# Optimization experiments

Measured on AMD Instinct MI355X. Metric: run time of the kernel, lower is better.

The kernel has to match this reference:

```python
import jax, jax.numpy as jnp
import numpy as np

H = 1024
E = 1024
B = 4096
DEPTH = 1


def setup_inputs() -> dict:
    key = jax.random.key(0)
    ks = jax.random.split(key, 12)
    s = 1.0 / np.sqrt(E + 2 * H)
    inp = {
        "X": jax.random.normal(ks[0], (B, E), jnp.float32),
        "index": 0,
        "length": 64,
        "prev_a": jax.random.normal(ks[1], (B, DEPTH + 1, H), jnp.float32),
        "prev_b": jax.random.normal(ks[2], (B, DEPTH + 1, H), jnp.float32),
        "prev_depth": jax.random.randint(ks[3], (B, 1), 0, 2, jnp.int32),
        # torch Linear weights: y = x @ W.T, W shape (out, in)
        "w_a00": jax.random.uniform(ks[4], (H, E + 2 * H), jnp.float32, -s, s),
        "w_a10": jax.random.uniform(ks[5], (H, E + H), jnp.float32, -s, s),
        "w_b00": jax.random.uniform(ks[6], (H, E + 2 * H), jnp.float32, -s, s),
        "w_b11": jax.random.uniform(ks[7], (H, E + H), jnp.float32, -s, s),
        "w_b10": jax.random.uniform(ks[8], (H, E + H), jnp.float32, -s, s),
        "w_b01": jax.random.uniform(ks[9], (H, E + 2 * H), jnp.float32, -s, s),
        "w_att": jax.random.uniform(ks[10], (4, 8 * H), jnp.float32, -s, s),
    }
    return inp


def _gate(pd, cond_val, branch, carry):
    # eq(pd,cond)*branch + gt(pd,cond)*carry + lt(pd,cond)*0
    eq = (pd == cond_val).astype(branch.dtype)
    gt = (pd > cond_val).astype(branch.dtype)
    return eq * branch + gt * carry


def reference(X, index, length, prev_a, prev_b, prev_depth,
              w_a00, w_a10, w_b00, w_b11, w_b10, w_b01, w_att):
    b, h = X.shape[0], prev_b.shape[-1]
    pd = prev_depth.astype(X.dtype)  # (B,1)
    a0, a1 = prev_a[:, 0, :], prev_a[:, 1, :]
    b0, b1 = prev_b[:, 0, :], prev_b[:, 1, :]

    # d = 1 (only depth level)
    nofork_nojoin_a = jnp.concatenate([X, b0, a1], 1) @ w_a00.T
    fork_nojoin_a = jnp.concatenate([X, b0], 1) @ w_a10.T
    na00 = _gate(pd, 1.0, nofork_nojoin_a, a1)
    na11 = _gate(pd, 1.0, a1, a1)                 # fork_join_a = prev_a[:,1]
    na10 = _gate(pd, 0.0, fork_nojoin_a, a1)      # eq(pd+1, 1) <=> pd == 0
    na01 = _gate(pd, 2.0, a0, a1)                 # eq(pd-1, 1) <=> pd == 2

    fork_join_b = jnp.concatenate([X, b1], 1) @ w_b11.T
    nofork_nojoin_b = jnp.concatenate([X, a1, na00], 1) @ w_b00.T
    fork_nojoin_b = jnp.concatenate([X, na10], 1) @ w_b10.T
    nofork_join_b = jnp.concatenate([X, b0, a1], 1) @ w_b01.T
    nb00 = _gate(pd, 1.0, nofork_nojoin_b, b1)
    nb11 = _gate(pd, 1.0, fork_join_b, b1)
    nb10 = _gate(pd, 0.0, fork_nojoin_b, b1)
    nb01 = _gate(pd, 2.0, nofork_join_b, b1)

    zeros2h = jnp.zeros((b, 2 * h), X.dtype)  # d=0 slot of each branch
    f00 = jnp.concatenate([zeros2h, na00, nb00], 1)  # (B, stride=4h)
    f01 = jnp.concatenate([zeros2h, na01, nb01], 1)
    f10 = jnp.concatenate([zeros2h, na10, nb10], 1)
    f11 = jnp.concatenate([zeros2h, na11, nb11], 1)
    state = jnp.stack([f00, f01, f10, f11], 1)  # (B, 4, 4h)

    # attention over next_state_flat[:, depth_size:] == [f10, f11]
    att_in = jnp.concatenate([f10, f11], 1)  # (B, 8h)
    pd0 = pd[:, 0]
    e0 = (pd0 == 0.0).astype(X.dtype)
    e1 = (pd0 == 1.0).astype(X.dtype)
    eD = (pd0 == float(DEPTH)).astype(X.dtype)
    mask = jnp.stack([1 - e0, (1 - e0) * (1 - e1), 1 - eD, 1 - e0], 1)  # (B,4)
    att_vars = mask * jax.nn.softmax(jax.nn.sigmoid(att_in @ w_att.T), axis=1)

    # straight-through argmax: forward one-hot, backward identity
    hard = jax.nn.one_hot(jnp.argmax(att_vars, axis=1), 4, dtype=X.dtype)
    sel = jax.lax.stop_gradient(hard - att_vars) + att_vars

    # bmm with striped identity == select the chosen stripe
    hidden = jnp.einsum('bk,bkd->bd', sel, state).reshape(b, DEPTH + 1, 2 * h)
    next_a = hidden[:, :, :h]
    next_b = hidden[:, :, h:]

    pdi = prev_depth[:, 0]
    hi = hard.astype(prev_depth.dtype)
    next_depth = (hi[:, 0] * pdi + hi[:, 1] * (pdi - 1)
                  + hi[:, 2] * (pdi + 1) + hi[:, 3] * pdi)[:, None]
    f = (sel[:, 2] + sel[:, 3])[:, None]
    j = (sel[:, 1] + sel[:, 3])[:, None]
    return (next_a, next_b, next_depth, f, j)
```

## Files before the change

### kernel.cpp

```cpp
#include <hip/hip_runtime.h>
#include <hip/hip_bf16.h>
#include <stdint.h>
#include <math.h>

typedef unsigned short u16;
typedef __attribute__((ext_vector_type(8))) short frag8;
typedef __attribute__((ext_vector_type(4))) float f32x4;

#define Hdim 1024
#define Brows 4096

#define OUT_B_OFF  8388608
#define OUT_D_OFF 16777216
#define OUT_F_OFF 16781312
#define OUT_J_OFF 16785408

#define XB      0u
#define B0B     4194304u
#define A1B     8388608u
#define B1B     12582912u
#define NA00B   16777216u
#define NA10B   20971520u
#define WA00B   25165824u
#define WA10B   28311552u
#define WB00B   30408704u
#define WB11B   33554432u
#define WB10B   35651584u
#define WS_BF_ELTS 37748736u
#define WS_NEED (32768ull + (unsigned long long)WS_BF_ELTS * 2ull)

#define NO_BCOPY 0xFFFFFFFFu

__device__ __forceinline__ u16 f2bf(float f) {
    union { float f; unsigned int i; } v; v.f = f;
    unsigned int r = v.i + 0x7fffu + ((v.i >> 16) & 1u);
    return (u16)(r >> 16);
}
__device__ __forceinline__ unsigned int pk2(float a, float b) {
    __hip_bfloat162 h = __float22bfloat162_rn(make_float2(a, b));
    union { __hip_bfloat162 h; unsigned int u; } v; v.h = h; return v.u;
}
__device__ __forceinline__ void gl_lds16(const u16* g, u16* l) {
    __builtin_amdgcn_global_load_lds(
        (const __attribute__((address_space(1))) unsigned int*)g,
        (__attribute__((address_space(3))) unsigned int*)l, 16, 0, 0);
}


struct GDesc {
    unsigned int a0, a1s, a2;
    unsigned int w;
    unsigned int bcopy;
    int K;
    int ksel;
    int pad;
    const int* gate;
    float* outp;
};
struct GPack { GDesc d[3]; };

__global__ __launch_bounds__(256)
void gemm_multi(u16* __restrict__ ws16, GPack gp)
{
    __shared__ alignas(16) u16 lsA[128 * 64];
    __shared__ alignas(16) u16 lsB[64 * 64];

    const GDesc g = gp.d[blockIdx.z];

    const int tid  = threadIdx.x;
    const int lane = tid & 63;
    const int wv   = tid >> 6;
    const int wm   = wv >> 1, wn = wv & 1;
    const int m0   = blockIdx.x * 128;
    const int n0   = blockIdx.y * 64;

    f32x4 acc[4][2];
#pragma unroll
    for (int i = 0; i < 4; ++i)
#pragma unroll
        for (int j = 0; j < 2; ++j) acc[i][j] = (f32x4){0.f, 0.f, 0.f, 0.f};

    const u16* segp[3] = { ws16 + g.a0, ws16 + g.a1s, ws16 + g.a2 };
    const u16* W = ws16 + g.w;
    const int K = g.K;

    const int nkt = K / 64;
    for (int kt = 0; kt < nkt; ++kt) {
        const int seg = kt >> 4;
        const int kl  = (kt & 15) * 64;
        const u16* ab = segp[seg] + (size_t)m0 * 1024 + kl;
        const u16* wb = W + (size_t)n0 * K + kt * 64;
#pragma unroll
        for (int i = 0; i < 4; ++i) {
            const int ch = i * 256 + tid;
            const int r = ch >> 3, c = ch & 7;
            gl_lds16(ab + (size_t)r * 1024 + ((c ^ (r & 7)) * 8), &lsA[ch * 8]);
        }
#pragma unroll
        for (int i = 0; i < 2; ++i) {
            const int ch = i * 256 + tid;
            const int r = ch >> 3, c = ch & 7;
            gl_lds16(wb + (size_t)r * K + ((c ^ (r & 7)) * 8), &lsB[ch * 8]);
        }
        __syncthreads();
#pragma unroll
        for (int ks = 0; ks < 2; ++ks) {
            const int kb = (ks * 32 + (lane >> 4) * 8) * 2;
            frag8 af[4], bfr[2];
#pragma unroll
            for (int i = 0; i < 4; ++i) {
                const int ro = wm * 64 + i * 16 + (lane & 15);
                af[i] = *(const frag8*)((const char*)lsA +
                            ((ro * 128 + kb) ^ ((ro & 7) << 4)));
            }
#pragma unroll
            for (int j = 0; j < 2; ++j) {
                const int ro = wn * 32 + j * 16 + (lane & 15);
                bfr[j] = *(const frag8*)((const char*)lsB +
                            ((ro * 128 + kb) ^ ((ro & 7) << 4)));
            }
#pragma unroll
            for (int i = 0; i < 4; ++i)
#pragma unroll
                for (int j = 0; j < 2; ++j)
                    acc[i][j] = __builtin_amdgcn_mfma_f32_16x16x32_bf16(af[i], bfr[j], acc[i][j], 0, 0, 0);
        }
        __syncthreads();
    }

    u16* bc = (g.bcopy != NO_BCOPY) ? (ws16 + g.bcopy) : nullptr;
    const int quad = lane >> 4;
    const int lcol = lane & 15;
#pragma unroll
    for (int i = 0; i < 4; ++i) {
#pragma unroll
        for (int r = 0; r < 4; ++r) {
            const int grow = m0 + wm * 64 + i * 16 + quad * 4 + r;
            const int gv = g.gate[grow];
#pragma unroll
            for (int j = 0; j < 2; ++j) {
                const int gcol = n0 + wn * 32 + j * 16 + lcol;
                const float v = acc[i][j][r];
                if (bc) bc[(size_t)grow * 1024 + gcol] = f2bf(v);
                if (gv == g.ksel) g.outp[(size_t)grow * 2048 + gcol] = v;
            }
        }
    }
}

__global__ __launch_bounds__(256)
void convert_all(const float* __restrict__ X,
                 const float* __restrict__ prev_a, const float* __restrict__ prev_b,
                 const float* __restrict__ wa00, const float* __restrict__ wa10,
                 const float* __restrict__ wb00, const float* __restrict__ wb11,
                 const float* __restrict__ wb10,
                 u16* __restrict__ ws16)
{
    long long gid = (long long)blockIdx.x * 256 + threadIdx.x;
    const float* src;
    unsigned int dst;
    long long idx;
    if (gid < 1048576) {
        idx = gid;               src = X + idx * 4;    dst = XB;
    } else if (gid < 1835008) {
        idx = gid - 1048576;     src = wa00 + idx * 4; dst = WA00B;
    } else if (gid < 2359296) {
        idx = gid - 1835008;     src = wa10 + idx * 4; dst = WA10B;
    } else if (gid < 3145728) {
        idx = gid - 2359296;     src = wb00 + idx * 4; dst = WB00B;
    } else if (gid < 3670016) {
        idx = gid - 3145728;     src = wb11 + idx * 4; dst = WB11B;
    } else if (gid < 4194304) {
        idx = gid - 3670016;     src = wb10 + idx * 4; dst = WB10B;
    } else if (gid < 5242880) {
        idx = gid - 4194304;
        src = prev_b + (idx >> 8) * 2048 + (idx & 255) * 4;          dst = B0B;
    } else if (gid < 6291456) {
        idx = gid - 5242880;
        src = prev_a + (idx >> 8) * 2048 + 1024 + (idx & 255) * 4;   dst = A1B;
    } else {
        idx = gid - 6291456;
        src = prev_b + (idx >> 8) * 2048 + 1024 + (idx & 255) * 4;   dst = B1B;
    }
    float4 v = *(const float4*)src;
    uint2 h = { pk2(v.x, v.y), pk2(v.z, v.w) };
    *(uint2*)&ws16[(size_t)dst + idx * 4] = h;
}

#define BMf 128
#define BNf 64
#define LDK 72

struct RegTile { float4 a[8]; float4 b[4]; };

__device__ __forceinline__ void load_tile(RegTile& s,
        const float* const* segp, const int* segs,
        const float* __restrict__ W, int K, int kn,
        int m0, int n0, int lr, int lc)
{
    const int seg = kn >> 4;
    const int kl  = (kn & 15) * 64;
    const float* ab = segp[seg];
    const int astr  = segs[seg];
#pragma unroll
    for (int i = 0; i < 8; ++i)
        s.a[i] = *(const float4*)(ab + (size_t)(m0 + i * 16 + lr) * astr + kl + lc);
#pragma unroll
    for (int i = 0; i < 4; ++i)
        s.b[i] = *(const float4*)(W + (size_t)(n0 + i * 16 + lr) * K + kn * 64 + lc);
}
__device__ __forceinline__ void stage_tile(const RegTile& s, u16* LA, u16* LB,
                                           int lr, int lc)
{
#pragma unroll
    for (int i = 0; i < 8; ++i) {
        uint2 h = { pk2(s.a[i].x, s.a[i].y), pk2(s.a[i].z, s.a[i].w) };
        *(uint2*)&LA[(i * 16 + lr) * LDK + lc] = h;
    }
#pragma unroll
    for (int i = 0; i < 4; ++i) {
        uint2 h = { pk2(s.b[i].x, s.b[i].y), pk2(s.b[i].z, s.b[i].w) };
        *(uint2*)&LB[(i * 16 + lr) * LDK + lc] = h;
    }
}
__device__ __forceinline__ void do_mfma_f(const u16* LA, const u16* LB,
                                          int wm, int wn, int lane, f32x4 acc[4][2])
{
#pragma unroll
    for (int ks = 0; ks < 2; ++ks) {
        const int kc = ks * 32 + (lane >> 4) * 8;
        frag8 af[4], bf[2];
#pragma unroll
        for (int i = 0; i < 4; ++i)
            af[i] = *(const frag8*)&LA[(wm * 64 + i * 16 + (lane & 15)) * LDK + kc];
#pragma unroll
        for (int j = 0; j < 2; ++j)
            bf[j] = *(const frag8*)&LB[(wn * 32 + j * 16 + (lane & 15)) * LDK + kc];
#pragma unroll
        for (int i = 0; i < 4; ++i)
#pragma unroll
            for (int j = 0; j < 2; ++j)
                acc[i][j] = __builtin_amdgcn_mfma_f32_16x16x32_bf16(af[i], bf[j], acc[i][j], 0, 0, 0);
    }
}

__global__ __launch_bounds__(256)
void gemm_k(const float* __restrict__ a0, int as0,
            const float* __restrict__ a1p, int as1,
            const float* __restrict__ a2p, int as2,
            const float* __restrict__ W, int K,
            const int* __restrict__ gate, int ksel,
            float* __restrict__ outp, int ostr)
{
    __shared__ alignas(16) u16 lsA[2][BMf * LDK];
    __shared__ alignas(16) u16 lsB[2][BNf * LDK];

    const int tid  = threadIdx.x;
    const int lane = tid & 63;
    const int wv   = tid >> 6;
    const int wm   = wv >> 1, wn = wv & 1;
    const int m0   = blockIdx.x * BMf;
    const int n0   = blockIdx.y * BNf;
    const int lr = tid >> 4;
    const int lc = (tid & 15) * 4;

    f32x4 acc[4][2];
#pragma unroll
    for (int i = 0; i < 4; ++i)
#pragma unroll
        for (int j = 0; j < 2; ++j) acc[i][j] = (f32x4){0.f, 0.f, 0.f, 0.f};

    const float* segp[3] = { a0, a1p, a2p };
    const int    segs[3] = { as0, as1, as2 };

    const int nkt = K / 64;
    RegTile S0, S1;
    load_tile(S0, segp, segs, W, K, 0, m0, n0, lr, lc);
    load_tile(S1, segp, segs, W, K, 1, m0, n0, lr, lc);
    stage_tile(S0, lsA[0], lsB[0], lr, lc);
    __syncthreads();

    for (int kt = 0; kt < nkt; kt += 2) {
        if (kt + 2 < nkt) load_tile(S0, segp, segs, W, K, kt + 2, m0, n0, lr, lc);
        do_mfma_f(lsA[0], lsB[0], wm, wn, lane, acc);
        stage_tile(S1, lsA[1], lsB[1], lr, lc);
        __syncthreads();
        if (kt + 3 < nkt) load_tile(S1, segp, segs, W, K, kt + 3, m0, n0, lr, lc);
        do_mfma_f(lsA[1], lsB[1], wm, wn, lane, acc);
        if (kt + 2 < nkt) {
            stage_tile(S0, lsA[0], lsB[0], lr, lc);
            __syncthreads();
        }
    }

    const int quad = lane >> 4;
    const int lcol = lane & 15;
#pragma unroll
    for (int i = 0; i < 4; ++i) {
#pragma unroll
        for (int r = 0; r < 4; ++r) {
            const int grow = m0 + wm * 64 + i * 16 + quad * 4 + r;
            if (gate[grow] == ksel) {
#pragma unroll
                for (int j = 0; j < 2; ++j) {
                    const int gcol = n0 + wn * 32 + j * 16 + lcol;
                    outp[(size_t)grow * ostr + gcol] = acc[i][j][r];
                }
            }
        }
    }
}

__global__ __launch_bounds__(256)
void prep_u(const float* __restrict__ w_b11, const float* __restrict__ w_att,
            float* __restrict__ u)
{
    const int k  = (blockIdx.x & 7) * 256 + threadIdx.x;
    const int c0 = (blockIdx.x >> 3) * 16;
    float s0 = 0.f, s3 = 0.f;
    for (int c = c0; c < c0 + 16; ++c) {
        const float w = w_b11[(size_t)c * 2048 + k];
        s0 += w * w_att[7168 + c];
        s3 += w * w_att[3 * 8192 + 7168 + c];
    }
    atomicAdd(&u[k], s0);
    atomicAdd(&u[2048 + k], s3);
}

__global__ __launch_bounds__(256)
void decide(const float* __restrict__ X,
            const float* __restrict__ prev_a, const float* __restrict__ prev_b,
            const int* __restrict__ pdin,
            const float* __restrict__ w_att,
            const float* __restrict__ u,
            int* __restrict__ kbuf,
            float* __restrict__ out)
{
    const int lane = threadIdx.x & 63;
    const int wv   = threadIdx.x >> 6;
    const int b    = blockIdx.x * 4 + wv;
    const int pd   = pdin[b];

    const float* a1 = prev_a + (size_t)b * 2048 + 1024;
    const float* b1 = prev_b + (size_t)b * 2048 + 1024;
    const float* xr = X + (size_t)b * 1024;

    int k;
    float fv;
    if (pd == 0) {
        k = 2; fv = 1.f;
    } else {
        float d0 = 0.f, d3 = 0.f;
        const float* w0 = w_att;
        const float* w3 = w_att + 3 * 8192;
        const float* u0 = u;
        const float* u3 = u + 2048;
#pragma unroll
        for (int uu = 0; uu < 2; ++uu) {
            const int c = lane * 16 + uu * 8;
#pragma unroll
            for (int q = 0; q < 2; ++q) {
                const int cc = c + q * 4;
                float4 av = *(const float4*)&a1[cc];
                float4 bv = *(const float4*)&b1[cc];
                float4 xv = *(const float4*)&xr[cc];
                float4 wa0 = *(const float4*)&w0[2048 + cc];
                float4 wb0 = *(const float4*)&w0[3072 + cc];
                float4 wc0 = *(const float4*)&w0[6144 + cc];
                float4 wa3 = *(const float4*)&w3[2048 + cc];
                float4 wb3 = *(const float4*)&w3[3072 + cc];
                float4 wc3 = *(const float4*)&w3[6144 + cc];
                float4 ux0 = *(const float4*)&u0[cc];
                float4 ux3 = *(const float4*)&u3[cc];
                float4 ub0 = *(const float4*)&u0[1024 + cc];
                float4 ub3 = *(const float4*)&u3[1024 + cc];
                d0 += av.x*(wa0.x+wc0.x) + av.y*(wa0.y+wc0.y) + av.z*(wa0.z+wc0.z) + av.w*(wa0.w+wc0.w);
                d3 += av.x*(wa3.x+wc3.x) + av.y*(wa3.y+wc3.y) + av.z*(wa3.z+wc3.z) + av.w*(wa3.w+wc3.w);
                d0 += bv.x*wb0.x + bv.y*wb0.y + bv.z*wb0.z + bv.w*wb0.w;
                d3 += bv.x*wb3.x + bv.y*wb3.y + bv.z*wb3.z + bv.w*wb3.w;
                d0 += xv.x*ux0.x + xv.y*ux0.y + xv.z*ux0.z + xv.w*ux0.w;
                d3 += xv.x*ux3.x + xv.y*ux3.y + xv.z*ux3.z + xv.w*ux3.w;
                d0 += bv.x*ub0.x + bv.y*ub0.y + bv.z*ub0.z + bv.w*ub0.w;
                d3 += bv.x*ub3.x + bv.y*ub3.y + bv.z*ub3.z + bv.w*ub3.w;
            }
        }
#pragma unroll
        for (int off = 32; off; off >>= 1) {
            d0 += __shfl_xor(d0, off, 64);
            d3 += __shfl_xor(d3, off, 64);
        }
        k = (d3 > d0) ? 3 : 0;
        fv = (k == 3) ? 1.f : 0.f;
    }
    const float jv = (pd == 0) ? 0.f : fv;
    const int nd = (k == 2) ? pd + 1 : pd;

    float* outA = out;
    float* outB = out + OUT_B_OFF;

    const float4 z4 = make_float4(0.f, 0.f, 0.f, 0.f);
#pragma unroll
    for (int uu = 0; uu < 4; ++uu) {
        const int c = lane * 16 + uu * 4;
        *(float4*)&outA[(size_t)b * 2048 + c] = z4;
        *(float4*)&outB[(size_t)b * 2048 + c] = z4;
    }
    if (k == 3) {
#pragma unroll
        for (int uu = 0; uu < 4; ++uu) {
            const int c = lane * 16 + uu * 4;
            *(float4*)&outA[(size_t)b * 2048 + 1024 + c] = *(const float4*)&a1[c];
        }
    }
    if (lane == 0) {
        kbuf[b] = k;
        out[OUT_D_OFF + b] = (float)nd;
        out[OUT_F_OFF + b] = fv;
        out[OUT_J_OFF + b] = jv;
    }
}

extern "C" void kernel_launch(void* const* d_in, const int* in_sizes, int n_in,
                              void* d_out, int out_size, void* d_ws, size_t ws_size,
                              hipStream_t stream)
{
    const float* X      = (const float*)d_in[0];
    const float* prev_a = (const float*)d_in[3];
    const float* prev_b = (const float*)d_in[4];
    const int*   pd     = (const int*)d_in[5];
    const float* w_a00  = (const float*)d_in[6];
    const float* w_a10  = (const float*)d_in[7];
    const float* w_b00  = (const float*)d_in[8];
    const float* w_b11  = (const float*)d_in[9];
    const float* w_b10  = (const float*)d_in[10];
    const float* w_att  = (const float*)d_in[12];

    float* u    = (float*)d_ws;
    int*   kbuf = (int*)((char*)d_ws + 16384);

    const float* a1 = prev_a + 1024;
    const float* b0 = prev_b;
    const float* b1 = prev_b + 1024;

    float* out   = (float*)d_out;
    float* outA1 = out + 1024;
    float* outB1 = out + OUT_B_OFF + 1024;

    dim3 blk(256);

    hipMemsetAsync(u, 0, 16384, stream);
    prep_u<<<dim3(512), blk, 0, stream>>>(w_b11, w_att, u);
    decide<<<dim3(Brows / 4), blk, 0, stream>>>(X, prev_a, prev_b, pd, w_att, u, kbuf, out);

    if (ws_size >= WS_NEED) {
        u16* ws16 = (u16*)((char*)d_ws + 32768);
        convert_all<<<dim3(28672), blk, 0, stream>>>(X, prev_a, prev_b,
            w_a00, w_a10, w_b00, w_b11, w_b10, ws16);

        GPack p1;
        p1.d[0] = { XB, B0B, A1B, WA00B, NA00B,    3072, 0, 0, kbuf, outA1 };
        p1.d[1] = { XB, B0B, 0u,  WA10B, NA10B,    2048, 2, 0, kbuf, outA1 };
        p1.d[2] = { XB, B1B, 0u,  WB11B, NO_BCOPY, 2048, 1, 0, pd,   outB1 };
        gemm_multi<<<dim3(Brows / 128, Hdim / 64, 3), blk, 0, stream>>>(ws16, p1);

        GPack p2;
        p2.d[0] = { XB, A1B,   NA00B, WB00B, NO_BCOPY, 3072, 0, 0, kbuf, outB1 };
        p2.d[1] = { XB, NA10B, 0u,    WB10B, NO_BCOPY, 2048, 2, 0, kbuf, outB1 };
        p2.d[2] = p2.d[0];
        gemm_multi<<<dim3(Brows / 128, Hdim / 64, 2), blk, 0, stream>>>(ws16, p2);
    } else {
        dim3 grid(Brows / BMf, Hdim / BNf);
        gemm_k<<<grid, blk, 0, stream>>>(X, 1024, b0, 2048, a1, 2048,
                                         w_a00, 3072, kbuf, 0, outA1, 2048);
        gemm_k<<<grid, blk, 0, stream>>>(X, 1024, b0, 2048, nullptr, 0,
                                         w_a10, 2048, kbuf, 2, outA1, 2048);
        gemm_k<<<grid, blk, 0, stream>>>(X, 1024, b1, 2048, nullptr, 0,
                                         w_b11, 2048, pd, 1, outB1, 2048);
        gemm_k<<<grid, blk, 0, stream>>>(X, 1024, a1, 2048, outA1, 2048,
                                         w_b00, 3072, kbuf, 0, outB1, 2048);
        gemm_k<<<grid, blk, 0, stream>>>(X, 1024, outA1, 2048, nullptr, 0,
                                         w_b10, 2048, kbuf, 2, outB1, 2048);
    }
}
```

Before: 362.5 us.

## Compact rows per selected branch and run gathered GEMMs only on them

```diff
diff --git a/kernel.cpp b/kernel.cpp
--- a/kernel.cpp
+++ b/kernel.cpp
@@ -14,6 +14,9 @@
 #define OUT_D_OFF 16777216
 #define OUT_F_OFF 16781312
 #define OUT_J_OFF 16785408
+
+#define LISTS_OFF 32768
+#define BF16_OFF  98304
 
 #define XB      0u
 #define B0B     4194304u
@@ -27,7 +30,7 @@
 #define WB11B   33554432u
 #define WB10B   35651584u
 #define WS_BF_ELTS 37748736u
-#define WS_NEED (32768ull + (unsigned long long)WS_BF_ELTS * 2ull)
+#define WS_NEED ((unsigned long long)BF16_OFF + (unsigned long long)WS_BF_ELTS * 2ull)
 
 #define NO_BCOPY 0xFFFFFFFFu
 
@@ -52,27 +55,33 @@
     unsigned int w;
     unsigned int bcopy;
     int K;
-    int ksel;
-    int pad;
-    const int* gate;
+    const int* rows;
     float* outp;
 };
 struct GPack { GDesc d[3]; };
 
 __global__ __launch_bounds__(256)
-void gemm_multi(u16* __restrict__ ws16, GPack gp)
+void gemm_gather(u16* __restrict__ ws16, GPack gp)
 {
     __shared__ alignas(16) u16 lsA[128 * 64];
     __shared__ alignas(16) u16 lsB[64 * 64];
 
     const GDesc g = gp.d[blockIdx.z];
+    const int m0 = blockIdx.x * 128;
+    if (g.rows[m0] < 0) return;
 
     const int tid  = threadIdx.x;
     const int lane = tid & 63;
     const int wv   = tid >> 6;
     const int wm   = wv >> 1, wn = wv & 1;
-    const int m0   = blockIdx.x * 128;
     const int n0   = blockIdx.y * 64;
+
+    int ridx[4];
+#pragma unroll
+    for (int i = 0; i < 4; ++i) {
+        const int rv = g.rows[m0 + (tid >> 3) + i * 32];
+        ridx[i] = rv < 0 ? 0 : rv;
+    }
 
     f32x4 acc[4][2];
 #pragma unroll
@@ -83,25 +92,22 @@
     const u16* segp[3] = { ws16 + g.a0, ws16 + g.a1s, ws16 + g.a2 };
     const u16* W = ws16 + g.w;
     const int K = g.K;
+
+    const int swz = ((tid & 7) ^ ((tid >> 3) & 7)) * 8;
+    const int brow0 = tid >> 3;
 
     const int nkt = K / 64;
     for (int kt = 0; kt < nkt; ++kt) {
         const int seg = kt >> 4;
         const int kl  = (kt & 15) * 64;
-        const u16* ab = segp[seg] + (size_t)m0 * 1024 + kl;
+        const u16* abase = segp[seg] + kl;
         const u16* wb = W + (size_t)n0 * K + kt * 64;
 #pragma unroll
-        for (int i = 0; i < 4; ++i) {
-            const int ch = i * 256 + tid;
-            const int r = ch >> 3, c = ch & 7;
-            gl_lds16(ab + (size_t)r * 1024 + ((c ^ (r & 7)) * 8), &lsA[ch * 8]);
-        }
-#pragma unroll
-        for (int i = 0; i < 2; ++i) {
-            const int ch = i * 256 + tid;
-            const int r = ch >> 3, c = ch & 7;
-            gl_lds16(wb + (size_t)r * K + ((c ^ (r & 7)) * 8), &lsB[ch * 8]);
-        }
+        for (int i = 0; i < 4; ++i)
+            gl_lds16(abase + (size_t)ridx[i] * 1024 + swz, &lsA[(i * 256 + tid) * 8]);
+#pragma unroll
+        for (int i = 0; i < 2; ++i)
+            gl_lds16(wb + (size_t)(i * 32 + brow0) * K + swz, &lsB[(i * 256 + tid) * 8]);
         __syncthreads();
 #pragma unroll
         for (int ks = 0; ks < 2; ++ks) {
@@ -135,16 +141,48 @@
     for (int i = 0; i < 4; ++i) {
 #pragma unroll
         for (int r = 0; r < 4; ++r) {
-            const int grow = m0 + wm * 64 + i * 16 + quad * 4 + r;
-            const int gv = g.gate[grow];
+            const int grow = g.rows[m0 + wm * 64 + i * 16 + quad * 4 + r];
+            if (grow < 0) continue;
 #pragma unroll
             for (int j = 0; j < 2; ++j) {
                 const int gcol = n0 + wn * 32 + j * 16 + lcol;
                 const float v = acc[i][j][r];
                 if (bc) bc[(size_t)grow * 1024 + gcol] = f2bf(v);
-                if (gv == g.ksel) g.outp[(size_t)grow * 2048 + gcol] = v;
+                g.outp[(size_t)grow * 2048 + gcol] = v;
             }
         }
+    }
+}
+
+__global__ __launch_bounds__(1024)
+void build_lists(const int* __restrict__ kbuf, int* __restrict__ lists)
+{
+    __shared__ int sc[1024];
+    const int t = threadIdx.x;
+    int ks[4];
+#pragma unroll
+    for (int i = 0; i < 4; ++i) ks[i] = kbuf[t * 4 + i];
+
+#pragma unroll
+    for (int j = 0; j < 3; ++j) {
+        const int kv = (j == 0) ? 0 : (j == 1) ? 2 : 3;
+        int c = 0;
+#pragma unroll
+        for (int i = 0; i < 4; ++i) c += (ks[i] == kv);
+        sc[t] = c;
+        __syncthreads();
+        for (int off = 1; off < 1024; off <<= 1) {
+            const int v = (t >= off) ? sc[t - off] : 0;
+            __syncthreads();
+            sc[t] += v;
+            __syncthreads();
+        }
+        int pos = sc[t] - c;
+        int* lst = lists + j * 4096;
+#pragma unroll
+        for (int i = 0; i < 4; ++i)
+            if (ks[i] == kv) lst[pos++] = t * 4 + i;
+        __syncthreads();
     }
 }
 
@@ -435,8 +473,9 @@
     const float* w_b10  = (const float*)d_in[10];
     const float* w_att  = (const float*)d_in[12];
 
-    float* u    = (float*)d_ws;
-    int*   kbuf = (int*)((char*)d_ws + 16384);
+    float* u     = (float*)d_ws;
+    int*   kbuf  = (int*)((char*)d_ws + 16384);
+    int*   lists = (int*)((char*)d_ws + LISTS_OFF);
 
     const float* a1 = prev_a + 1024;
     const float* b0 = prev_b;
@@ -453,21 +492,28 @@
     decide<<<dim3(Brows / 4), blk, 0, stream>>>(X, prev_a, prev_b, pd, w_att, u, kbuf, out);
 
     if (ws_size >= WS_NEED) {
-        u16* ws16 = (u16*)((char*)d_ws + 32768);
+        hipMemsetAsync(lists, 0xFF, 3 * 4096 * sizeof(int), stream);
+        build_lists<<<dim3(1), dim3(1024), 0, stream>>>(kbuf, lists);
+
+        u16* ws16 = (u16*)((char*)d_ws + BF16_OFF);
         convert_all<<<dim3(28672), blk, 0, stream>>>(X, prev_a, prev_b,
             w_a00, w_a10, w_b00, w_b11, w_b10, ws16);
 
+        int* l0 = lists;
+        int* l2 = lists + 4096;
+        int* l3 = lists + 8192;
+
         GPack p1;
-        p1.d[0] = { XB, B0B, A1B, WA00B, NA00B,    3072, 0, 0, kbuf, outA1 };
-        p1.d[1] = { XB, B0B, 0u,  WA10B, NA10B,    2048, 2, 0, kbuf, outA1 };
-        p1.d[2] = { XB, B1B, 0u,  WB11B, NO_BCOPY, 2048, 1, 0, pd,   outB1 };
-        gemm_multi<<<dim3(Brows / 128, Hdim / 64, 3), blk, 0, stream>>>(ws16, p1);
+        p1.d[0] = { XB, B0B, A1B, WA00B, NA00B,    3072, l0, outA1 };
+        p1.d[1] = { XB, B0B, 0u,  WA10B, NA10B,    2048, l2, outA1 };
+        p1.d[2] = { XB, B1B, 0u,  WB11B, NO_BCOPY, 2048, l3, outB1 };
+        gemm_gather<<<dim3(Brows / 128, Hdim / 64, 3), blk, 0, stream>>>(ws16, p1);
 
         GPack p2;
-        p2.d[0] = { XB, A1B,   NA00B, WB00B, NO_BCOPY, 3072, 0, 0, kbuf, outB1 };
-        p2.d[1] = { XB, NA10B, 0u,    WB10B, NO_BCOPY, 2048, 2, 0, kbuf, outB1 };
+        p2.d[0] = { XB, A1B,   NA00B, WB00B, NO_BCOPY, 3072, l0, outB1 };
+        p2.d[1] = { XB, NA10B, 0u,    WB10B, NO_BCOPY, 2048, l2, outB1 };
         p2.d[2] = p2.d[0];
-        gemm_multi<<<dim3(Brows / 128, Hdim / 64, 2), blk, 0, stream>>>(ws16, p2);
+        gemm_gather<<<dim3(Brows / 128, Hdim / 64, 2), blk, 0, stream>>>(ws16, p2);
     } else {
         dim3 grid(Brows / BMf, Hdim / BNf);
         gemm_k<<<grid, blk, 0, stream>>>(X, 1024, b0, 2048, a1, 2048,
```

Result: no change. 365.4 us (+0.8%).
